# Performance work log

Hardware: AMD Instinct MI355X
Metric: run time of the kernel (lower is better)

The kernel has to match this reference:

```python
import jax, jax.numpy as jnp
import numpy as np

B = 262144
L, NO, NW = 5, 5, 3          # num_layers, num_ops, num_widths
AD = L * NO * NW             # arch_dim = 75
D, H = 64, 4                 # embed_dim, num_heads
HD = D // H                  # head_dim = 16
EPS = 1e-5


def _ln(x, g, b):
    m = x.mean(-1, keepdims=True)
    v = ((x - m) ** 2).mean(-1, keepdims=True)
    return (x - m) / jnp.sqrt(v + EPS) * g + b


def setup_inputs() -> dict:
    key = jax.random.key(0)
    ks = jax.random.split(key, 16)
    s = 0.05
    return {
        "hw_idx": jax.random.randint(ks[0], (B,), 0, 4),
        "op_indices": jax.random.randint(ks[1], (B, L), 0, NO),
        "width_indices": jax.random.randint(ks[2], (B, L), 0, NW),
        "hw_embed": jax.random.normal(ks[3], (4, D)) * s,
        "W1": jax.random.normal(ks[4], (128, AD)) * s, "b1": jnp.zeros((128,)),
        "W2": jax.random.normal(ks[5], (D, 128)) * s, "b2": jnp.zeros((D,)),
        "ln1_g": jnp.ones((D,)), "ln1_b": jnp.zeros((D,)),
        "in_proj_w": jax.random.normal(ks[6], (3 * D, D)) * s,
        "in_proj_b": jnp.zeros((3 * D,)),
        "out_proj_w": jax.random.normal(ks[7], (D, D)) * s,
        "out_proj_b": jnp.zeros((D,)),
        "ln2_g": jnp.ones((D,)), "ln2_b": jnp.zeros((D,)),
        "W3": jax.random.normal(ks[8], (32, D)) * s, "b3": jnp.zeros((32,)),
        "W4": jax.random.normal(ks[9], (1, 32)) * s, "b4": jnp.zeros((1,)),
    }


def reference(hw_idx, op_indices, width_indices, hw_embed, W1, b1, W2, b2,
              ln1_g, ln1_b, in_proj_w, in_proj_b, out_proj_w, out_proj_b,
              ln2_g, ln2_b, W3, b3, W4, b4):
    # hardware embedding lookup -> [B, D]
    hw_emb = hw_embed[hw_idx]
    # vectorized one-hot arch encoding: [B, L*NO*NW]
    cell = op_indices * NW + width_indices                  # [B, L]
    onehot = jax.nn.one_hot(cell, NO * NW, dtype=jnp.float32).reshape(-1, AD)
    # arch encoder MLP + LayerNorm (dropout = identity at eval)
    h = jax.nn.relu(onehot @ W1.T + b1)
    arch_emb = _ln(h @ W2.T + b2, ln1_g, ln1_b)             # [B, D]
    # combined sequence of 2 tokens: [B, 2, D]
    combined = jnp.stack([hw_emb, arch_emb], axis=1)
    # multi-head self-attention (torch MultiheadAttention, batch_first)
    qkv = combined @ in_proj_w.T + in_proj_b                # [B, 2, 3D]
    q, k, v = jnp.split(qkv, 3, axis=-1)
    q = q.reshape(-1, 2, H, HD); k = k.reshape(-1, 2, H, HD); v = v.reshape(-1, 2, H, HD)
    scores = jnp.einsum('bqhd,bkhd->bhqk', q, k) / np.sqrt(HD)
    attn = jax.nn.softmax(scores, axis=-1)
    ctx = jnp.einsum('bhqk,bkhd->bqhd', attn, v).reshape(-1, 2, D)
    attn_out = ctx @ out_proj_w.T + out_proj_b
    # residual + LayerNorm, mean-pool over the 2 tokens
    x = _ln(attn_out + combined, ln2_g, ln2_b)
    pooled = x.mean(axis=1)                                 # [B, D]
    # prediction head
    latency = jax.nn.relu(pooled @ W3.T + b3) @ W4.T + b4   # [B, 1]
    return latency
```

## Files before the change

### kernel.cpp

```cpp
#include <hip/hip_runtime.h>


using s8v = __attribute__((ext_vector_type(8))) short;
using h8  = __attribute__((ext_vector_type(8))) _Float16;
using f4  = __attribute__((ext_vector_type(4))) float;

#define BTOT 262144

#define WF_W1   0
#define WF_W2   12288
#define WF_IP   20480
#define WF_OP   32768
#define WF_W3   36864
#define WF_HWE  38912

#define OF_POOL 2304
#define OF_ARCH 3456
#define PWS     4608

__device__ __forceinline__ unsigned short f2h(float f) {
  _Float16 h = (_Float16)f;
  return __builtin_bit_cast(unsigned short, h);
}

__device__ __forceinline__ void swz(const float* __restrict__ W,
                                    const float* __restrict__ bias,
                                    unsigned short* __restrict__ dst,
                                    int Kreal, int KS, int NT, int t, int stride) {
  const int total = KS * NT * 512;
  for (int i = t; i < total; i += stride) {
    const int j = i & 7, ln = (i >> 3) & 63, fr = i >> 9;
    const int nt = fr % NT, ks = fr / NT;
    const int n = nt * 16 + (ln & 15);
    const int k = ks * 32 + (ln >> 4) * 8 + j;
    float v = 0.f;
    if (k < Kreal) v = W[n * Kreal + k];
    else if (bias && k == Kreal) v = bias[n];
    dst[i] = f2h(v);
  }
}

__global__ void k_pre(const float* __restrict__ hwe,
                      const float* __restrict__ W1, const float* __restrict__ b1,
                      const float* __restrict__ W2,
                      const float* __restrict__ ipw, const float* __restrict__ opw,
                      const float* __restrict__ W3,
                      unsigned short* __restrict__ ws) {
  const int t = blockIdx.x * 256 + threadIdx.x;
  const int stride = gridDim.x * 256;
  swz(W1,  b1,      ws + WF_W1, 75, 3, 8, t, stride);
  swz(W2,  nullptr, ws + WF_W2, 128, 4, 4, t, stride);
  swz(ipw, nullptr, ws + WF_IP, 64, 2, 12, t, stride);
  swz(opw, nullptr, ws + WF_OP, 64, 2, 4, t, stride);
  swz(W3,  nullptr, ws + WF_W3, 64, 2, 2, t, stride);
  for (int i = t; i < 256; i += stride) ws[WF_HWE + i] = f2h(hwe[i]);
}

__global__ __launch_bounds__(256, 4) void k_fused(
    const int* __restrict__ g_hw,
    const int* __restrict__ g_op, const int* __restrict__ g_wd,
    const float* __restrict__ g_hwe,
    const float* __restrict__ g_b2,
    const float* __restrict__ g_ln1g, const float* __restrict__ g_ln1b,
    const float* __restrict__ g_ipb, const float* __restrict__ g_opb,
    const float* __restrict__ g_ln2g, const float* __restrict__ g_ln2b,
    const float* __restrict__ g_b3,  const float* __restrict__ g_W4,
    const float* __restrict__ g_b4,
    const unsigned short* __restrict__ wsf,
    float* __restrict__ g_out) {
  __shared__ __align__(16) unsigned short sm[4 * PWS];
  const int tid = threadIdx.x;
  const int wave = tid >> 6, lane = tid & 63;
  const int quad = lane >> 4, l15 = lane & 15;
  unsigned short* pw = sm + wave * PWS;
  const int m0 = (blockIdx.x * 4 + wave) * 16;

  int hwv = 0, c0 = 0, c1 = 0, c2 = 0, c3 = 0, c4 = 0;
  if (lane < 16) {
    const int smp = m0 + lane;
    hwv = g_hw[smp];
    c0 =      g_op[smp * 5 + 0] * 3 + g_wd[smp * 5 + 0];
    c1 = 15 + g_op[smp * 5 + 1] * 3 + g_wd[smp * 5 + 1];
    c2 = 30 + g_op[smp * 5 + 2] * 3 + g_wd[smp * 5 + 2];
    c3 = 45 + g_op[smp * 5 + 3] * 3 + g_wd[smp * 5 + 3];
    c4 = 60 + g_op[smp * 5 + 4] * 3 + g_wd[smp * 5 + 4];
  }
  const int t0 = __shfl(c0, l15), t1 = __shfl(c1, l15), t2 = __shfl(c2, l15);
  const int t3 = __shfl(c3, l15), t4 = __shfl(c4, l15);
  const int hwrow = __shfl(hwv, l15);

  float b2v[4], l1gv[4], l1bv[4], opbv[4], l2gv[4], l2bv[4];
#pragma unroll
  for (int nt = 0; nt < 4; ++nt) {
    const int col = nt * 16 + l15;
    b2v[nt] = g_b2[col];  l1gv[nt] = g_ln1g[col]; l1bv[nt] = g_ln1b[col];
    opbv[nt] = g_opb[col]; l2gv[nt] = g_ln2g[col]; l2bv[nt] = g_ln2b[col];
  }
  float ipbv[12];
#pragma unroll
  for (int nt = 0; nt < 12; ++nt) ipbv[nt] = g_ipb[nt * 16 + l15];
  float b3v[2], w4vv[2];
#pragma unroll
  for (int nt = 0; nt < 2; ++nt) {
    b3v[nt] = g_b3[nt * 16 + l15];
    w4vv[nt] = g_W4[nt * 16 + l15];
  }
  const float b4v = g_b4[0];

  h8 aoh[3];
#pragma unroll
  for (int ks = 0; ks < 3; ++ks) {
    s8v a;
#pragma unroll
    for (int j = 0; j < 8; ++j) {
      const int k = ks * 32 + quad * 8 + j;
      const bool hit = (k == 75) || (k == t0) || (k == t1) || (k == t2) ||
                       (k == t3) || (k == t4);
      a[j] = hit ? (short)0x3C00 : (short)0;
    }
    aoh[ks] = __builtin_bit_cast(h8, a);
  }

#pragma unroll
  for (int nt = 0; nt < 8; ++nt) {
    f4 acc = {0.f, 0.f, 0.f, 0.f};
#pragma unroll
    for (int ks = 0; ks < 3; ++ks) {
      const h8 bf = *(const h8*)(wsf + WF_W1 + ((ks * 8 + nt) * 64 + lane) * 8);
      acc = __builtin_amdgcn_mfma_f32_16x16x32_f16(aoh[ks], bf, acc, 0, 0, 0);
    }
    const int col = nt * 16 + l15;
#pragma unroll
    for (int r = 0; r < 4; ++r) {
      float v = acc[r];
      v = v > 0.f ? v : 0.f;
      pw[(quad * 4 + r) * 136 + col] = f2h(v);
    }
  }

  h8 a2[4];
#pragma unroll
  for (int ks = 0; ks < 4; ++ks)
    a2[ks] = *(const h8*)(pw + l15 * 136 + ks * 32 + quad * 8);
  float archres[4][4];
  {
    float val[4][4];
#pragma unroll
    for (int nt = 0; nt < 4; ++nt) {
      f4 acc = {0.f, 0.f, 0.f, 0.f};
#pragma unroll
      for (int ks = 0; ks < 4; ++ks) {
        const h8 bf = *(const h8*)(wsf + WF_W2 + ((ks * 4 + nt) * 64 + lane) * 8);
        acc = __builtin_amdgcn_mfma_f32_16x16x32_f16(a2[ks], bf, acc, 0, 0, 0);
      }
#pragma unroll
      for (int r = 0; r < 4; ++r) val[nt][r] = acc[r] + b2v[nt];
    }
#pragma unroll
    for (int r = 0; r < 4; ++r) {
      float s = val[0][r] + val[1][r] + val[2][r] + val[3][r];
      float q = val[0][r] * val[0][r] + val[1][r] * val[1][r] +
                val[2][r] * val[2][r] + val[3][r] * val[3][r];
#pragma unroll
      for (int off = 1; off <= 8; off <<= 1) {
        s += __shfl_xor(s, off);
        q += __shfl_xor(q, off);
      }
      const float mean = s * (1.f / 64.f);
      const float var  = q * (1.f / 64.f) - mean * mean;
      const float rstd = rsqrtf(var + 1e-5f);
#pragma unroll
      for (int nt = 0; nt < 4; ++nt) {
        const int col = nt * 16 + l15;
        const float xn = (val[nt][r] - mean) * rstd * l1gv[nt] + l1bv[nt];
        archres[nt][r] = xn;
        pw[OF_ARCH + (quad * 4 + r) * 72 + col] = f2h(xn);
      }
    }
  }

  h8 at0[2], at1[2];
#pragma unroll
  for (int ks = 0; ks < 2; ++ks) {
    at0[ks] = *(const h8*)(wsf + WF_HWE + hwrow * 64 + ks * 32 + quad * 8);
    at1[ks] = *(const h8*)(pw + OF_ARCH + l15 * 72 + ks * 32 + quad * 8);
  }
#pragma unroll
  for (int h = 0; h < 4; ++h) {
    f4 aq0 = {0.f,0.f,0.f,0.f}, aq1 = {0.f,0.f,0.f,0.f};
    f4 ak0 = {0.f,0.f,0.f,0.f}, ak1 = {0.f,0.f,0.f,0.f};
    f4 av0 = {0.f,0.f,0.f,0.f}, av1 = {0.f,0.f,0.f,0.f};
#pragma unroll
    for (int ks = 0; ks < 2; ++ks) {
      const h8 bq = *(const h8*)(wsf + WF_IP + ((ks * 12 + h    ) * 64 + lane) * 8);
      const h8 bk = *(const h8*)(wsf + WF_IP + ((ks * 12 + h + 4) * 64 + lane) * 8);
      const h8 bv = *(const h8*)(wsf + WF_IP + ((ks * 12 + h + 8) * 64 + lane) * 8);
      aq0 = __builtin_amdgcn_mfma_f32_16x16x32_f16(at0[ks], bq, aq0, 0, 0, 0);
      aq1 = __builtin_amdgcn_mfma_f32_16x16x32_f16(at1[ks], bq, aq1, 0, 0, 0);
      ak0 = __builtin_amdgcn_mfma_f32_16x16x32_f16(at0[ks], bk, ak0, 0, 0, 0);
      ak1 = __builtin_amdgcn_mfma_f32_16x16x32_f16(at1[ks], bk, ak1, 0, 0, 0);
      av0 = __builtin_amdgcn_mfma_f32_16x16x32_f16(at0[ks], bv, av0, 0, 0, 0);
      av1 = __builtin_amdgcn_mfma_f32_16x16x32_f16(at1[ks], bv, av1, 0, 0, 0);
    }
    float d0[4], d1[4], v0[4], v1[4];
#pragma unroll
    for (int r = 0; r < 4; ++r) {
      const float dk = (ak1[r] + ipbv[h + 4]) - (ak0[r] + ipbv[h + 4]);
      d0[r] = (aq0[r] + ipbv[h]) * dk;
      d1[r] = (aq1[r] + ipbv[h]) * dk;
      v0[r] = av0[r] + ipbv[h + 8];
      v1[r] = av1[r] + ipbv[h + 8];
    }
#pragma unroll
    for (int off = 1; off <= 8; off <<= 1)
#pragma unroll
      for (int r = 0; r < 4; ++r) {
        d0[r] += __shfl_xor(d0[r], off);
        d1[r] += __shfl_xor(d1[r], off);
      }
#pragma unroll
    for (int r = 0; r < 4; ++r) {
      const float dsc0 = d0[r] * 0.25f, dsc1 = d1[r] * 0.25f;
      const float g0 = fmaxf(dsc0, 0.f);
      const float e01 = __expf(dsc0 - g0), e00 = __expf(-g0);
      const float i0 = 1.f / (e00 + e01);
      const float g1 = fmaxf(dsc1, 0.f);
      const float e11 = __expf(dsc1 - g1), e10 = __expf(-g1);
      const float i1 = 1.f / (e10 + e11);
      const float ctx0 = (e00 * i0) * v0[r] + (e01 * i0) * v1[r];
      const float ctx1 = (e10 * i1) * v0[r] + (e11 * i1) * v1[r];
      const int col = h * 16 + l15;
      pw[(quad * 4 + r) * 72 + col]        = f2h(ctx0);
      pw[(16 + quad * 4 + r) * 72 + col]   = f2h(ctx1);
    }
  }

  h8 ca[2][2];
#pragma unroll
  for (int mt = 0; mt < 2; ++mt)
#pragma unroll
    for (int ks = 0; ks < 2; ++ks)
      ca[mt][ks] = *(const h8*)(pw + (mt * 16 + l15) * 72 + ks * 32 + quad * 8);
  f4 oacc[2][4];
#pragma unroll
  for (int nt = 0; nt < 4; ++nt) {
    const h8 bf0 = *(const h8*)(wsf + WF_OP + ((0 * 4 + nt) * 64 + lane) * 8);
    const h8 bf1 = *(const h8*)(wsf + WF_OP + ((1 * 4 + nt) * 64 + lane) * 8);
#pragma unroll
    for (int mt = 0; mt < 2; ++mt) {
      f4 acc = {0.f, 0.f, 0.f, 0.f};
      acc = __builtin_amdgcn_mfma_f32_16x16x32_f16(ca[mt][0], bf0, acc, 0, 0, 0);
      acc = __builtin_amdgcn_mfma_f32_16x16x32_f16(ca[mt][1], bf1, acc, 0, 0, 0);
      oacc[mt][nt] = acc;
    }
  }
  float pool[4][4];
#pragma unroll
  for (int mt = 0; mt < 2; ++mt) {
    float val[4][4];
#pragma unroll
    for (int r = 0; r < 4; ++r) {
      if (mt == 0) {
        const int hr = __shfl(hwv, quad * 4 + r);
#pragma unroll
        for (int nt = 0; nt < 4; ++nt)
          val[nt][r] = oacc[0][nt][r] + opbv[nt] + g_hwe[hr * 64 + nt * 16 + l15];
      } else {
#pragma unroll
        for (int nt = 0; nt < 4; ++nt)
          val[nt][r] = oacc[1][nt][r] + opbv[nt] + archres[nt][r];
      }
    }
#pragma unroll
    for (int r = 0; r < 4; ++r) {
      float s = val[0][r] + val[1][r] + val[2][r] + val[3][r];
      float q = val[0][r] * val[0][r] + val[1][r] * val[1][r] +
                val[2][r] * val[2][r] + val[3][r] * val[3][r];
#pragma unroll
      for (int off = 1; off <= 8; off <<= 1) {
        s += __shfl_xor(s, off);
        q += __shfl_xor(q, off);
      }
      const float mean = s * (1.f / 64.f);
      const float var  = q * (1.f / 64.f) - mean * mean;
      const float rstd = rsqrtf(var + 1e-5f);
#pragma unroll
      for (int nt = 0; nt < 4; ++nt) {
        const float xn = (val[nt][r] - mean) * rstd * l2gv[nt] + l2bv[nt];
        if (mt == 0) pool[nt][r] = 0.5f * xn;
        else         pool[nt][r] += 0.5f * xn;
      }
    }
  }
#pragma unroll
  for (int nt = 0; nt < 4; ++nt)
#pragma unroll
    for (int r = 0; r < 4; ++r)
      pw[OF_POOL + (quad * 4 + r) * 72 + nt * 16 + l15] = f2h(pool[nt][r]);

  h8 pa[2];
#pragma unroll
  for (int ks = 0; ks < 2; ++ks)
    pa[ks] = *(const h8*)(pw + OF_POOL + l15 * 72 + ks * 32 + quad * 8);
  float part[4] = {0.f, 0.f, 0.f, 0.f};
#pragma unroll
  for (int nt = 0; nt < 2; ++nt) {
    const h8 bf0 = *(const h8*)(wsf + WF_W3 + ((0 * 2 + nt) * 64 + lane) * 8);
    const h8 bf1 = *(const h8*)(wsf + WF_W3 + ((1 * 2 + nt) * 64 + lane) * 8);
    f4 acc = {0.f, 0.f, 0.f, 0.f};
    acc = __builtin_amdgcn_mfma_f32_16x16x32_f16(pa[0], bf0, acc, 0, 0, 0);
    acc = __builtin_amdgcn_mfma_f32_16x16x32_f16(pa[1], bf1, acc, 0, 0, 0);
#pragma unroll
    for (int r = 0; r < 4; ++r) {
      float y = acc[r] + b3v[nt];
      y = y > 0.f ? y : 0.f;
      part[r] += y * w4vv[nt];
    }
  }
#pragma unroll
  for (int off = 1; off <= 8; off <<= 1)
#pragma unroll
    for (int r = 0; r < 4; ++r)
      part[r] += __shfl_xor(part[r], off);
  if (l15 == 0) {
#pragma unroll
    for (int r = 0; r < 4; ++r)
      g_out[m0 + quad * 4 + r] = part[r] + b4v;
  }
}

extern "C" void kernel_launch(void* const* d_in, const int* in_sizes, int n_in,
                              void* d_out, int out_size, void* d_ws, size_t ws_size,
                              hipStream_t stream) {
  (void)in_sizes; (void)n_in; (void)out_size; (void)ws_size;
  unsigned short* ws = (unsigned short*)d_ws;

  k_pre<<<64, 256, 0, stream>>>(
      (const float*)d_in[3], (const float*)d_in[4], (const float*)d_in[5],
      (const float*)d_in[6], (const float*)d_in[10], (const float*)d_in[12],
      (const float*)d_in[16], ws);

  k_fused<<<4096, 256, 0, stream>>>(
      (const int*)d_in[0],
      (const int*)d_in[1], (const int*)d_in[2],
      (const float*)d_in[3],
      (const float*)d_in[7],
      (const float*)d_in[8], (const float*)d_in[9],
      (const float*)d_in[11], (const float*)d_in[13],
      (const float*)d_in[14], (const float*)d_in[15],
      (const float*)d_in[17], (const float*)d_in[18],
      (const float*)d_in[19],
      ws, (float*)d_out);
}
```

Baseline: 176.0 us.

## Alias per-wave LDS regions, raise occupancy target, simplify 2-token softmax

Arch-embedding, context and pooled tiles now share one LDS scratch region per wave, halving the shared-memory footprint. Launch bounds rise from 4 to 8 blocks per CU so more waves can be resident. The two-key softmax becomes a sigmoid with a lerp, and the key bias is dropped because it cancels in the key difference. The cost is a register cap of about 64 VGPRs at the new bound, which may force spills given the many per-thread bias and accumulator arrays.

```diff
diff --git a/kernel.cpp b/kernel.cpp
--- a/kernel.cpp
+++ b/kernel.cpp
@@ -4,8 +4,6 @@
 using s8v = __attribute__((ext_vector_type(8))) short;
 using h8  = __attribute__((ext_vector_type(8))) _Float16;
 using f4  = __attribute__((ext_vector_type(4))) float;
-
-#define BTOT 262144
 
 #define WF_W1   0
 #define WF_W2   12288
@@ -14,9 +12,7 @@
 #define WF_W3   36864
 #define WF_HWE  38912
 
-#define OF_POOL 2304
-#define OF_ARCH 3456
-#define PWS     4608
+#define PWS     2304
 
 __device__ __forceinline__ unsigned short f2h(float f) {
   _Float16 h = (_Float16)f;
@@ -56,7 +52,7 @@
   for (int i = t; i < 256; i += stride) ws[WF_HWE + i] = f2h(hwe[i]);
 }
 
-__global__ __launch_bounds__(256, 4) void k_fused(
+__global__ __launch_bounds__(256, 8) void k_fused(
     const int* __restrict__ g_hw,
     const int* __restrict__ g_op, const int* __restrict__ g_wd,
     const float* __restrict__ g_hwe,
@@ -96,9 +92,12 @@
     b2v[nt] = g_b2[col];  l1gv[nt] = g_ln1g[col]; l1bv[nt] = g_ln1b[col];
     opbv[nt] = g_opb[col]; l2gv[nt] = g_ln2g[col]; l2bv[nt] = g_ln2b[col];
   }
-  float ipbv[12];
-#pragma unroll
-  for (int nt = 0; nt < 12; ++nt) ipbv[nt] = g_ipb[nt * 16 + l15];
+  float ipbq[4], ipbvv[4];
+#pragma unroll
+  for (int h = 0; h < 4; ++h) {
+    ipbq[h]  = g_ipb[h * 16 + l15];
+    ipbvv[h] = g_ipb[(h + 8) * 16 + l15];
+  }
   float b3v[2], w4vv[2];
 #pragma unroll
   for (int nt = 0; nt < 2; ++nt) {
@@ -174,7 +173,7 @@
         const int col = nt * 16 + l15;
         const float xn = (val[nt][r] - mean) * rstd * l1gv[nt] + l1bv[nt];
         archres[nt][r] = xn;
-        pw[OF_ARCH + (quad * 4 + r) * 72 + col] = f2h(xn);
+        pw[(quad * 4 + r) * 72 + col] = f2h(xn);
       }
     }
   }
@@ -183,7 +182,7 @@
 #pragma unroll
   for (int ks = 0; ks < 2; ++ks) {
     at0[ks] = *(const h8*)(wsf + WF_HWE + hwrow * 64 + ks * 32 + quad * 8);
-    at1[ks] = *(const h8*)(pw + OF_ARCH + l15 * 72 + ks * 32 + quad * 8);
+    at1[ks] = *(const h8*)(pw + l15 * 72 + ks * 32 + quad * 8);
   }
 #pragma unroll
   for (int h = 0; h < 4; ++h) {
@@ -205,11 +204,11 @@
     float d0[4], d1[4], v0[4], v1[4];
 #pragma unroll
     for (int r = 0; r < 4; ++r) {
-      const float dk = (ak1[r] + ipbv[h + 4]) - (ak0[r] + ipbv[h + 4]);
-      d0[r] = (aq0[r] + ipbv[h]) * dk;
-      d1[r] = (aq1[r] + ipbv[h]) * dk;
-      v0[r] = av0[r] + ipbv[h + 8];
-      v1[r] = av1[r] + ipbv[h + 8];
+      const float dk = ak1[r] - ak0[r];
+      d0[r] = (aq0[r] + ipbq[h]) * dk;
+      d1[r] = (aq1[r] + ipbq[h]) * dk;
+      v0[r] = av0[r] + ipbvv[h];
+      v1[r] = av1[r] + ipbvv[h];
     }
 #pragma unroll
     for (int off = 1; off <= 8; off <<= 1)
@@ -220,18 +219,14 @@
       }
 #pragma unroll
     for (int r = 0; r < 4; ++r) {
-      const float dsc0 = d0[r] * 0.25f, dsc1 = d1[r] * 0.25f;
-      const float g0 = fmaxf(dsc0, 0.f);
-      const float e01 = __expf(dsc0 - g0), e00 = __expf(-g0);
-      const float i0 = 1.f / (e00 + e01);
-      const float g1 = fmaxf(dsc1, 0.f);
-      const float e11 = __expf(dsc1 - g1), e10 = __expf(-g1);
-      const float i1 = 1.f / (e10 + e11);
-      const float ctx0 = (e00 * i0) * v0[r] + (e01 * i0) * v1[r];
-      const float ctx1 = (e10 * i1) * v0[r] + (e11 * i1) * v1[r];
+      const float a01 = 1.f / (1.f + __expf(-d0[r] * 0.25f));
+      const float a11 = 1.f / (1.f + __expf(-d1[r] * 0.25f));
+      const float dv = v1[r] - v0[r];
+      const float ctx0 = v0[r] + a01 * dv;
+      const float ctx1 = v0[r] + a11 * dv;
       const int col = h * 16 + l15;
-      pw[(quad * 4 + r) * 72 + col]        = f2h(ctx0);
-      pw[(16 + quad * 4 + r) * 72 + col]   = f2h(ctx1);
+      pw[(quad * 4 + r) * 72 + col]      = f2h(ctx0);
+      pw[(16 + quad * 4 + r) * 72 + col] = f2h(ctx1);
     }
   }
 
@@ -296,12 +291,12 @@
   for (int nt = 0; nt < 4; ++nt)
 #pragma unroll
     for (int r = 0; r < 4; ++r)
-      pw[OF_POOL + (quad * 4 + r) * 72 + nt * 16 + l15] = f2h(pool[nt][r]);
+      pw[(quad * 4 + r) * 72 + nt * 16 + l15] = f2h(pool[nt][r]);
 
   h8 pa[2];
 #pragma unroll
   for (int ks = 0; ks < 2; ++ks)
-    pa[ks] = *(const h8*)(pw + OF_POOL + l15 * 72 + ks * 32 + quad * 8);
+    pa[ks] = *(const h8*)(pw + l15 * 72 + ks * 32 + quad * 8);
   float part[4] = {0.f, 0.f, 0.f, 0.f};
 #pragma unroll
   for (int nt = 0; nt < 2; ++nt) {
```

Result: slower. 272.1 us (+54.6%).
